# Optimization experiments

Measured on AMD Instinct MI355X. Metric: run time of the kernel, lower is better.

## Reference

```python
import jax, jax.numpy as jnp
import numpy as np

B, T, C, H = 2, 2048, 1024, 16
WINDOW = 512
SOFTCAP = 30.0


def setup_inputs() -> dict:
    key = jax.random.key(0)
    ks = jax.random.split(key, 4)
    s = 0.02
    return {
        "x": jax.random.normal(ks[0], (B, T, C), dtype=jnp.float32),
        "suffix_prefix_length": jax.random.randint(ks[1], (B,), 0, 256),
        "W_qkv": jax.random.normal(ks[2], (3 * C, C), dtype=jnp.float32) * s,
        "b_qkv": jnp.zeros((3 * C,), dtype=jnp.float32),
        "W_proj": jax.random.normal(ks[3], (C, C), dtype=jnp.float32) * s,
        "b_proj": jnp.zeros((C,), dtype=jnp.float32),
    }


def reference(x, suffix_prefix_length, W_qkv, b_qkv, W_proj, b_proj):
    Bb, Tt, Cc = x.shape
    d = Cc // H
    # fused qkv projection (torch Linear: x @ W.T + b)
    qkv = x @ W_qkv.T + b_qkv
    q, k, v = jnp.split(qkv, 3, axis=-1)
    q = q.reshape(Bb, Tt, H, d).transpose(0, 2, 1, 3)  # [B,H,T,d]
    k = k.reshape(Bb, Tt, H, d).transpose(0, 2, 1, 3)
    v = v.reshape(Bb, Tt, H, d).transpose(0, 2, 1, 3)

    scale = 1.0 / np.sqrt(d).astype(np.float32)
    scores = jnp.einsum("bhqd,bhkd->bhqk", q, k) * scale
    # tanh softcap applied to unmasked scores (flex_attention score_mod path)
    scores = jnp.tanh(scores / SOFTCAP) * SOFTCAP

    qi = jnp.arange(Tt)[:, None]
    kj = jnp.arange(Tt)[None, :]
    sliding_causal = (qi >= kj) & (qi - kj <= WINDOW)          # [T,T]
    prefix_global = kj[None, :, :] < suffix_prefix_length[:, None, None]  # [B,T,T]
    mask = sliding_causal[None, None, :, :] | prefix_global[:, None, :, :]

    scores = jnp.where(mask, scores, -jnp.inf)
    att = jax.nn.softmax(scores, axis=-1)
    y = jnp.einsum("bhqk,bhkd->bhqd", att, v)
    y = y.transpose(0, 2, 1, 3).reshape(Bb, Tt, Cc)
    return y @ W_proj.T + b_proj
```

## Files before the change

kernel.cpp:

```cpp
#include <hip/hip_runtime.h>
#include <hip/hip_bf16.h>

typedef __bf16 bf16x8 __attribute__((ext_vector_type(8)));
typedef float f32x4 __attribute__((ext_vector_type(4)));

#define DEVI __device__ __forceinline__

constexpr int B_ = 2, T_ = 2048, C_ = 1024, H_ = 16, D_ = 64;
constexpr int M_ = B_ * T_;
constexpr int K_ = C_;
constexpr int WINDOW_ = 512;

DEVI unsigned short f2bf(float f) {
  return __builtin_bit_cast(unsigned short, (__bf16)f);
}

DEVI void gl_lds16(const unsigned short* g, unsigned short* l) {
  __builtin_amdgcn_global_load_lds(
      (const __attribute__((address_space(1))) unsigned int*)g,
      (__attribute__((address_space(3))) unsigned int*)l, 16, 0, 0);
}

__global__ void cvt_all(const float* __restrict__ x, const float* __restrict__ wqkv,
                        const float* __restrict__ wproj,
                        unsigned short* __restrict__ xb,
                        unsigned short* __restrict__ wqkvb,
                        unsigned short* __restrict__ wprojb) {
  constexpr int N1 = M_ * K_ / 4, N2 = 3 * C_ * K_ / 4, N3 = C_ * K_ / 4;
  int i = blockIdx.x * blockDim.x + threadIdx.x;
  const float* in;
  unsigned short* out;
  int idx;
  if (i < N1) { in = x; out = xb; idx = i; }
  else if (i < N1 + N2) { in = wqkv; out = wqkvb; idx = i - N1; }
  else if (i < N1 + N2 + N3) { in = wproj; out = wprojb; idx = i - N1 - N2; }
  else return;
  float4 v = reinterpret_cast<const float4*>(in)[idx];
  ushort4 o;
  o.x = f2bf(v.x); o.y = f2bf(v.y); o.z = f2bf(v.z); o.w = f2bf(v.w);
  reinterpret_cast<ushort4*>(out)[idx] = o;
}

template <int WHICH>
__global__ __launch_bounds__(256) void gemm_bt(
    const unsigned short* __restrict__ A, const unsigned short* __restrict__ W,
    const float* __restrict__ bias,
    unsigned short* __restrict__ oq, unsigned short* __restrict__ ok,
    unsigned short* __restrict__ ov, float* __restrict__ of) {
  __shared__ alignas(16) unsigned short As[128 * 32];
  __shared__ alignas(16) unsigned short Bs[128 * 32];

  const int tid = threadIdx.x;
  const int n0 = blockIdx.x * 128, m0 = blockIdx.y * 128;
  const int lane = tid & 63, w = tid >> 6;
  const int wm = (w >> 1) * 64, wn = (w & 1) * 64;
  const int lr = lane & 15, lg = lane >> 4;
  const int srow = lane >> 2, scs = (lane & 3) << 3;

  f32x4 acc[4][4];
#pragma unroll
  for (int i = 0; i < 4; i++)
#pragma unroll
    for (int j = 0; j < 4; j++) acc[i][j] = f32x4{0.f, 0.f, 0.f, 0.f};

  for (int kt = 0; kt < K_; kt += 32) {
#pragma unroll
    for (int i = 0; i < 2; i++) {
      const int rb = i * 64 + w * 16;
      gl_lds16(&A[(size_t)(m0 + rb + srow) * K_ + kt + scs], &As[rb * 32]);
      gl_lds16(&W[(size_t)(n0 + rb + srow) * K_ + kt + scs], &Bs[rb * 32]);
    }
    __syncthreads();
    bf16x8 af[4], bfr[4];
#pragma unroll
    for (int m = 0; m < 4; m++)
      af[m] = *reinterpret_cast<const bf16x8*>(&As[(wm + m * 16 + lr) * 32 + lg * 8]);
#pragma unroll
    for (int n = 0; n < 4; n++)
      bfr[n] = *reinterpret_cast<const bf16x8*>(&Bs[(wn + n * 16 + lr) * 32 + lg * 8]);
#pragma unroll
    for (int m = 0; m < 4; m++)
#pragma unroll
      for (int n = 0; n < 4; n++)
        acc[m][n] = __builtin_amdgcn_mfma_f32_16x16x32_bf16(af[m], bfr[n], acc[m][n], 0, 0, 0);
    __syncthreads();
  }

#pragma unroll
  for (int ms = 0; ms < 4; ms++) {
#pragma unroll
    for (int ns = 0; ns < 4; ns++) {
#pragma unroll
      for (int r = 0; r < 4; r++) {
        int m = m0 + wm + ms * 16 + lg * 4 + r;
        int n = n0 + wn + ns * 16 + lr;
        if constexpr (WHICH == 0) {
          float v = acc[ms][ns][r] + bias[n];
          int part = n >> 10, nc = n & 1023;
          int hh = nc >> 6, dd = nc & 63;
          int bb = m >> 11, tt = m & 2047;
          unsigned short bv = f2bf(v);
          size_t addr = (((size_t)(bb * H_ + hh)) * T_ + tt) * D_ + dd;
          if (part == 0) oq[addr] = bv;
          else if (part == 1) ok[addr] = bv;
          else ov[addr] = bv;
        } else {
          of[(size_t)m * C_ + n] = acc[ms][ns][r] + bias[n];
        }
      }
    }
  }
}

__global__ __launch_bounds__(256) void attn_fwd(
    const unsigned short* __restrict__ qg, const unsigned short* __restrict__ kg,
    const unsigned short* __restrict__ vg, const int* __restrict__ spl_arr,
    unsigned short* __restrict__ out) {
  const int tid = threadIdx.x;
  const int l = tid & 63, w = tid >> 6;
  const int lr = l & 15, lg = l >> 4;

  constexpr float C1 = 0.012022458674074695f;
  constexpr float C3 = -86.56170245333781f;

  const int lin = blockIdx.x;
  const int xs = lin & 7, slot = lin >> 3;
  const int g = xs + 8 * (slot >> 5);
  const int iblk = slot & 31;
  const int b = g >> 4, h = g & 15;
  const int q_base = iblk * 64;
  const int i0 = q_base + w * 16;

  const int spl = spl_arr[b];
  const size_t bh = (size_t)(b * H_ + h);
  const unsigned short* qp = qg + bh * T_ * D_;
  const unsigned short* kp = kg + bh * T_ * D_;
  const unsigned short* vp = vg + bh * T_ * D_;

  __shared__ alignas(16) unsigned short Ks[64 * 64];
  __shared__ alignas(16) unsigned short Vs[64 * 64];
  __shared__ alignas(16) unsigned short Ps[4][16][80];

  bf16x8 aq0 = *reinterpret_cast<const bf16x8*>(qp + (size_t)(i0 + lr) * D_ + lg * 8);
  bf16x8 aq1 = *reinterpret_cast<const bf16x8*>(qp + (size_t)(i0 + lr) * D_ + 32 + lg * 8);

  const unsigned short one_bf = 0x3F80;
  bf16x8 ONES;
#pragma unroll
  for (int i = 0; i < 8; i++) ONES[i] = __builtin_bit_cast(__bf16, one_bf);

  f32x4 acc[4];
  f32x4 accl = f32x4{0.f, 0.f, 0.f, 0.f};
#pragma unroll
  for (int nb = 0; nb < 4; nb++) acc[nb] = f32x4{0.f, 0.f, 0.f, 0.f};

  const int pref_tiles = (spl + 63) >> 6;
  const int pref_end = pref_tiles << 6;
  int wl = q_base - WINDOW_; if (wl < 0) wl = 0; wl &= ~63;
  const int start2 = wl > pref_end ? wl : pref_end;
  const int hi = q_base + 63;
  const int n2 = (start2 <= hi) ? (((hi - start2) >> 6) + 1) : 0;
  const int ntot = pref_tiles + n2;

  const int strow = tid >> 2;
  const int c0 = (tid & 3) << 4;
  const int ssw = (strow & 7) << 3;

  for (int tb = 0; tb < ntot; tb++) {
    const int j0 = (tb < pref_tiles) ? (tb << 6) : (start2 + ((tb - pref_tiles) << 6));
    {
      const unsigned short* krow = kp + (size_t)(j0 + strow) * D_;
      int4 ka0 = *reinterpret_cast<const int4*>(krow + c0);
      int4 ka1 = *reinterpret_cast<const int4*>(krow + c0 + 8);
      *reinterpret_cast<int4*>(&Ks[strow * 64 + (c0 ^ ssw)]) = ka0;
      *reinterpret_cast<int4*>(&Ks[strow * 64 + ((c0 + 8) ^ ssw)]) = ka1;
      union { int4 v4[2]; unsigned short u[16]; } vv;
      const unsigned short* vrow = vp + (size_t)(j0 + l) * D_ + w * 16;
      vv.v4[0] = *reinterpret_cast<const int4*>(vrow);
      vv.v4[1] = *reinterpret_cast<const int4*>(vrow + 8);
#pragma unroll
      for (int e = 0; e < 16; e++) {
        const int d = w * 16 + e;
        Vs[d * 64 + (l ^ ((d & 7) << 3))] = vv.u[e];
      }
    }
    __syncthreads();

    const bool rel = (j0 < spl) || (j0 + 63 >= i0 - WINDOW_ && j0 <= i0 + 15);
    if (rel) {
      f32x4 s[4];
#pragma unroll
      for (int ks = 0; ks < 4; ks++) {
        const int krow = ks * 16 + lr;
        const int sw = (krow & 7) << 3;
        bf16x8 b0 = *reinterpret_cast<const bf16x8*>(&Ks[krow * 64 + ((lg * 8) ^ sw)]);
        bf16x8 b1 = *reinterpret_cast<const bf16x8*>(&Ks[krow * 64 + ((32 + lg * 8) ^ sw)]);
        f32x4 t = f32x4{0.f, 0.f, 0.f, 0.f};
        t = __builtin_amdgcn_mfma_f32_16x16x32_bf16(aq0, b0, t, 0, 0, 0);
        s[ks] = __builtin_amdgcn_mfma_f32_16x16x32_bf16(aq1, b1, t, 0, 0, 0);
      }

      const bool fullv = (j0 + 63 < spl) ||
                         ((j0 + 63 <= i0) && (i0 + 15 - j0 <= WINDOW_));
      if (fullv) {
#pragma unroll
        for (int r = 0; r < 4; r++) {
          const int prow = lg * 4 + r;
#pragma unroll
          for (int ks = 0; ks < 4; ks++) {
            float t = __builtin_amdgcn_exp2f(s[ks][r] * C1);
            float p = __builtin_amdgcn_exp2f(C3 * __builtin_amdgcn_rcpf(1.0f + t));
            Ps[w][prow][ks * 16 + lr] = f2bf(p);
          }
        }
      } else {
#pragma unroll
        for (int r = 0; r < 4; r++) {
          const int prow = lg * 4 + r;
          const int irow = i0 + prow;
#pragma unroll
          for (int ks = 0; ks < 4; ks++) {
            const int jc = j0 + ks * 16 + lr;
            float t = __builtin_amdgcn_exp2f(s[ks][r] * C1);
            float p = __builtin_amdgcn_exp2f(C3 * __builtin_amdgcn_rcpf(1.0f + t));
            bool valid = (jc <= irow && irow - jc <= WINDOW_) || (jc < spl);
            p = valid ? p : 0.0f;
            Ps[w][prow][ks * 16 + lr] = f2bf(p);
          }
        }
      }

      asm volatile("s_waitcnt lgkmcnt(0)" ::: "memory");

      bf16x8 pa0 = *reinterpret_cast<const bf16x8*>(&Ps[w][lr][lg * 8]);
      bf16x8 pa1 = *reinterpret_cast<const bf16x8*>(&Ps[w][lr][32 + lg * 8]);

      accl = __builtin_amdgcn_mfma_f32_16x16x32_bf16(pa0, ONES, accl, 0, 0, 0);
      accl = __builtin_amdgcn_mfma_f32_16x16x32_bf16(pa1, ONES, accl, 0, 0, 0);

#pragma unroll
      for (int nb = 0; nb < 4; nb++) {
        const int vrow = nb * 16 + lr;
        const int sw = (vrow & 7) << 3;
        bf16x8 bv0 = *reinterpret_cast<const bf16x8*>(&Vs[vrow * 64 + ((lg * 8) ^ sw)]);
        bf16x8 bv1 = *reinterpret_cast<const bf16x8*>(&Vs[vrow * 64 + ((32 + lg * 8) ^ sw)]);
        acc[nb] = __builtin_amdgcn_mfma_f32_16x16x32_bf16(pa0, bv0, acc[nb], 0, 0, 0);
        acc[nb] = __builtin_amdgcn_mfma_f32_16x16x32_bf16(pa1, bv1, acc[nb], 0, 0, 0);
      }
    }
    __syncthreads();
  }

  float rl[4];
#pragma unroll
  for (int r = 0; r < 4; r++) rl[r] = __builtin_amdgcn_rcpf(accl[r]);
#pragma unroll
  for (int nb = 0; nb < 4; nb++) {
#pragma unroll
    for (int r = 0; r < 4; r++) {
      float o = acc[nb][r] * rl[r];
      int t = i0 + lg * 4 + r;
      out[((size_t)(b * T_ + t)) * C_ + h * D_ + nb * 16 + lr] = f2bf(o);
    }
  }
}

extern "C" void kernel_launch(void* const* d_in, const int* in_sizes, int n_in,
                              void* d_out, int out_size, void* d_ws, size_t ws_size,
                              hipStream_t stream) {
  const float* x = (const float*)d_in[0];
  const int* spl = (const int*)d_in[1];
  const float* Wqkv = (const float*)d_in[2];
  const float* bqkv = (const float*)d_in[3];
  const float* Wproj = (const float*)d_in[4];
  const float* bproj = (const float*)d_in[5];
  float* out = (float*)d_out;

  char* ws = (char*)d_ws;
  unsigned short* xb = (unsigned short*)ws;       ws += (size_t)M_ * K_ * 2;
  unsigned short* wqkvb = (unsigned short*)ws;    ws += (size_t)3 * C_ * K_ * 2;
  unsigned short* wprojb = (unsigned short*)ws;   ws += (size_t)C_ * K_ * 2;
  unsigned short* qb = (unsigned short*)ws;       ws += (size_t)M_ * C_ * 2;
  unsigned short* kb = (unsigned short*)ws;       ws += (size_t)M_ * C_ * 2;
  unsigned short* vb = (unsigned short*)ws;       ws += (size_t)M_ * C_ * 2;
  unsigned short* ab = (unsigned short*)ws;       ws += (size_t)M_ * C_ * 2;

  {
    constexpr int NT = (M_ * K_ + 3 * C_ * K_ + C_ * K_) / 4;
    cvt_all<<<(NT + 255) / 256, 256, 0, stream>>>(x, Wqkv, Wproj, xb, wqkvb, wprojb);
  }

  gemm_bt<0><<<dim3(3072 / 128, M_ / 128), 256, 0, stream>>>(
      xb, wqkvb, bqkv, qb, kb, vb, nullptr);

  attn_fwd<<<dim3(1024), 256, 0, stream>>>(qb, kb, vb, spl, ab);

  gemm_bt<1><<<dim3(C_ / 128, M_ / 128), 256, 0, stream>>>(
      ab, wprojb, bproj, nullptr, nullptr, nullptr, out);
}
```

Before: 178.2 us.

## Replace GEMM with 256x256 double-buffered tile kernel using swizzled LDS

Replaces the 128x128, K=32 single-buffered GEMM with a 512-thread kernel. Each block computes a 256x256 tile with a K step of 64, and LDS is double-buffered so the next tile loads while the current one is multiplied, using explicit vmcnt waits. LDS columns are XOR-swizzled to avoid bank conflicts, and the block index is remapped to improve L2 locality. The larger tiles raise data reuse per block but shrink the grid to 192 and 64 blocks, which leaves many CUs idle, especially for the output projection. The 128KB of LDS also limits each CU to one block.

Measured after the change: 187.3 us. 1.05x slower.

```diff
diff --git a/kernel.cpp b/kernel.cpp
--- a/kernel.cpp
+++ b/kernel.cpp
@@ -42,60 +42,101 @@
 }
 
 template <int WHICH>
-__global__ __launch_bounds__(256) void gemm_bt(
+__global__ __launch_bounds__(512, 2) void gemm256(
     const unsigned short* __restrict__ A, const unsigned short* __restrict__ W,
     const float* __restrict__ bias,
     unsigned short* __restrict__ oq, unsigned short* __restrict__ ok,
     unsigned short* __restrict__ ov, float* __restrict__ of) {
-  __shared__ alignas(16) unsigned short As[128 * 32];
-  __shared__ alignas(16) unsigned short Bs[128 * 32];
+  constexpr int NK = K_ / 64;
+  __shared__ alignas(16) unsigned short Al[2][256 * 64];
+  __shared__ alignas(16) unsigned short Bl[2][256 * 64];
 
   const int tid = threadIdx.x;
-  const int n0 = blockIdx.x * 128, m0 = blockIdx.y * 128;
   const int lane = tid & 63, w = tid >> 6;
-  const int wm = (w >> 1) * 64, wn = (w & 1) * 64;
+
+  const int nbx = gridDim.x;
+  const int nwg = nbx * 16;
+  const int orig = blockIdx.y * nbx + blockIdx.x;
+  const int cpx = nwg >> 3;
+  const int swz = (orig & 7) * cpx + (orig >> 3);
+  const int m0 = (swz & 15) * 256;
+  const int n0 = (swz >> 4) * 256;
+
+  const int wm = (w >> 2) * 128;
+  const int wn = (w & 3) * 64;
   const int lr = lane & 15, lg = lane >> 4;
-  const int srow = lane >> 2, scs = (lane & 3) << 3;
-
-  f32x4 acc[4][4];
-#pragma unroll
-  for (int i = 0; i < 4; i++)
+
+  const int srow8 = lane >> 3;
+  const int scol = ((lane & 7) ^ srow8) << 3;
+
+  f32x4 acc[8][4];
+#pragma unroll
+  for (int i = 0; i < 8; i++)
 #pragma unroll
     for (int j = 0; j < 4; j++) acc[i][j] = f32x4{0.f, 0.f, 0.f, 0.f};
 
-  for (int kt = 0; kt < K_; kt += 32) {
-#pragma unroll
-    for (int i = 0; i < 2; i++) {
-      const int rb = i * 64 + w * 16;
-      gl_lds16(&A[(size_t)(m0 + rb + srow) * K_ + kt + scs], &As[rb * 32]);
-      gl_lds16(&W[(size_t)(n0 + rb + srow) * K_ + kt + scs], &Bs[rb * 32]);
-    }
-    __syncthreads();
-    bf16x8 af[4], bfr[4];
-#pragma unroll
-    for (int m = 0; m < 4; m++)
-      af[m] = *reinterpret_cast<const bf16x8*>(&As[(wm + m * 16 + lr) * 32 + lg * 8]);
-#pragma unroll
-    for (int n = 0; n < 4; n++)
-      bfr[n] = *reinterpret_cast<const bf16x8*>(&Bs[(wn + n * 16 + lr) * 32 + lg * 8]);
-#pragma unroll
-    for (int m = 0; m < 4; m++)
-#pragma unroll
-      for (int n = 0; n < 4; n++)
-        acc[m][n] = __builtin_amdgcn_mfma_f32_16x16x32_bf16(af[m], bfr[n], acc[m][n], 0, 0, 0);
-    __syncthreads();
-  }
-
-#pragma unroll
-  for (int ms = 0; ms < 4; ms++) {
-#pragma unroll
-    for (int ns = 0; ns < 4; ns++) {
+  auto ISSUE = [&](int kt, int b) {
+#pragma unroll
+    for (int i = 0; i < 4; i++) {
+      const int row = i * 64 + w * 8 + srow8;
+      gl_lds16(&A[(size_t)(m0 + row) * K_ + kt * 64 + scol],
+               &Al[b][(i * 64 + w * 8) * 64]);
+    }
+#pragma unroll
+    for (int i = 0; i < 4; i++) {
+      const int row = i * 64 + w * 8 + srow8;
+      gl_lds16(&W[(size_t)(n0 + row) * K_ + kt * 64 + scol],
+               &Bl[b][(i * 64 + w * 8) * 64]);
+    }
+  };
+
+  ISSUE(0, 0);
+  ISSUE(1, 1);
+
+  for (int kt = 0; kt < NK; kt++) {
+    const int b = kt & 1;
+    if (kt + 1 < NK) asm volatile("s_waitcnt vmcnt(8)" ::: "memory");
+    else             asm volatile("s_waitcnt vmcnt(0)" ::: "memory");
+    __builtin_amdgcn_s_barrier();
+
+    bf16x8 bfrag[4][2];
+#pragma unroll
+    for (int nf = 0; nf < 4; nf++)
+#pragma unroll
+      for (int ks = 0; ks < 2; ks++) {
+        const int row = wn + nf * 16 + lr;
+        const int c16 = (ks * 4 + lg) ^ (row & 7);
+        bfrag[nf][ks] = *reinterpret_cast<const bf16x8*>(&Bl[b][row * 64 + c16 * 8]);
+      }
+#pragma unroll
+    for (int mf = 0; mf < 8; mf++) {
+      const int row = wm + mf * 16 + lr;
+      const int c0 = (0 * 4 + lg) ^ (row & 7);
+      const int c1 = (1 * 4 + lg) ^ (row & 7);
+      bf16x8 af0 = *reinterpret_cast<const bf16x8*>(&Al[b][row * 64 + c0 * 8]);
+      bf16x8 af1 = *reinterpret_cast<const bf16x8*>(&Al[b][row * 64 + c1 * 8]);
+#pragma unroll
+      for (int nf = 0; nf < 4; nf++) {
+        acc[mf][nf] = __builtin_amdgcn_mfma_f32_16x16x32_bf16(af0, bfrag[nf][0], acc[mf][nf], 0, 0, 0);
+        acc[mf][nf] = __builtin_amdgcn_mfma_f32_16x16x32_bf16(af1, bfrag[nf][1], acc[mf][nf], 0, 0, 0);
+      }
+    }
+
+    asm volatile("s_waitcnt lgkmcnt(0)" ::: "memory");
+    __builtin_amdgcn_s_barrier();
+    if (kt + 2 < NK) ISSUE(kt + 2, b);
+  }
+
+#pragma unroll
+  for (int mf = 0; mf < 8; mf++) {
+#pragma unroll
+    for (int nf = 0; nf < 4; nf++) {
 #pragma unroll
       for (int r = 0; r < 4; r++) {
-        int m = m0 + wm + ms * 16 + lg * 4 + r;
-        int n = n0 + wn + ns * 16 + lr;
+        const int m = m0 + wm + mf * 16 + lg * 4 + r;
+        const int n = n0 + wn + nf * 16 + lr;
         if constexpr (WHICH == 0) {
-          float v = acc[ms][ns][r] + bias[n];
+          float v = acc[mf][nf][r] + bias[n];
           int part = n >> 10, nc = n & 1023;
           int hh = nc >> 6, dd = nc & 63;
           int bb = m >> 11, tt = m & 2047;
@@ -105,7 +146,7 @@
           else if (part == 1) ok[addr] = bv;
           else ov[addr] = bv;
         } else {
-          of[(size_t)m * C_ + n] = acc[ms][ns][r] + bias[n];
+          of[(size_t)m * C_ + n] = acc[mf][nf][r] + bias[n];
         }
       }
     }
@@ -290,11 +331,11 @@
     cvt_all<<<(NT + 255) / 256, 256, 0, stream>>>(x, Wqkv, Wproj, xb, wqkvb, wprojb);
   }
 
-  gemm_bt<0><<<dim3(3072 / 128, M_ / 128), 256, 0, stream>>>(
+  gemm256<0><<<dim3(3072 / 256, M_ / 256), 512, 0, stream>>>(
       xb, wqkvb, bqkv, qb, kb, vb, nullptr);
 
   attn_fwd<<<dim3(1024), 256, 0, stream>>>(qb, kb, vb, spl, ab);
 
-  gemm_bt<1><<<dim3(C_ / 128, M_ / 128), 256, 0, stream>>>(
+  gemm256<1><<<dim3(C_ / 256, M_ / 256), 512, 0, stream>>>(
       ab, wprojb, bproj, nullptr, nullptr, nullptr, out);
 }
```

## Double GEMM K-tile with XOR-swizzled LDS and pack V transpose stores

Applied to the files above, without the earlier changes.

The projection GEMM now stages 64-wide K tiles instead of 32, halving the number of barrier pairs per K loop, and XOR-swizzles the LDS layout so fragment reads avoid bank conflicts. In the attention kernel, each thread loads two adjacent V rows and writes packed 32-bit pairs into the transposed V tile, replacing the scalar 16-bit scattered stores. This doubles GEMM LDS usage, which may reduce occupancy.

New measurement: 187.5 us. 1.05x slower.

```diff
diff --git a/kernel.cpp b/kernel.cpp
--- a/kernel.cpp
+++ b/kernel.cpp
@@ -47,15 +47,17 @@
     const float* __restrict__ bias,
     unsigned short* __restrict__ oq, unsigned short* __restrict__ ok,
     unsigned short* __restrict__ ov, float* __restrict__ of) {
-  __shared__ alignas(16) unsigned short As[128 * 32];
-  __shared__ alignas(16) unsigned short Bs[128 * 32];
+  __shared__ alignas(16) unsigned short As[128 * 64];
+  __shared__ alignas(16) unsigned short Bs[128 * 64];
 
   const int tid = threadIdx.x;
   const int n0 = blockIdx.x * 128, m0 = blockIdx.y * 128;
   const int lane = tid & 63, w = tid >> 6;
   const int wm = (w >> 1) * 64, wn = (w & 1) * 64;
   const int lr = lane & 15, lg = lane >> 4;
-  const int srow = lane >> 2, scs = (lane & 3) << 3;
+
+  const int srow = lane >> 3;
+  const int scol = ((lane & 7) ^ srow) << 3;
 
   f32x4 acc[4][4];
 #pragma unroll
@@ -63,26 +65,41 @@
 #pragma unroll
     for (int j = 0; j < 4; j++) acc[i][j] = f32x4{0.f, 0.f, 0.f, 0.f};
 
-  for (int kt = 0; kt < K_; kt += 32) {
-#pragma unroll
-    for (int i = 0; i < 2; i++) {
-      const int rb = i * 64 + w * 16;
-      gl_lds16(&A[(size_t)(m0 + rb + srow) * K_ + kt + scs], &As[rb * 32]);
-      gl_lds16(&W[(size_t)(n0 + rb + srow) * K_ + kt + scs], &Bs[rb * 32]);
+  for (int kt = 0; kt < K_; kt += 64) {
+#pragma unroll
+    for (int i = 0; i < 4; i++) {
+      const int rb = i * 32 + w * 8;
+      gl_lds16(&A[(size_t)(m0 + rb + srow) * K_ + kt + scol], &As[rb * 64]);
+    }
+#pragma unroll
+    for (int i = 0; i < 4; i++) {
+      const int rb = i * 32 + w * 8;
+      gl_lds16(&W[(size_t)(n0 + rb + srow) * K_ + kt + scol], &Bs[rb * 64]);
     }
     __syncthreads();
-    bf16x8 af[4], bfr[4];
-#pragma unroll
-    for (int m = 0; m < 4; m++)
-      af[m] = *reinterpret_cast<const bf16x8*>(&As[(wm + m * 16 + lr) * 32 + lg * 8]);
-#pragma unroll
-    for (int n = 0; n < 4; n++)
-      bfr[n] = *reinterpret_cast<const bf16x8*>(&Bs[(wn + n * 16 + lr) * 32 + lg * 8]);
-#pragma unroll
-    for (int m = 0; m < 4; m++)
-#pragma unroll
-      for (int n = 0; n < 4; n++)
-        acc[m][n] = __builtin_amdgcn_mfma_f32_16x16x32_bf16(af[m], bfr[n], acc[m][n], 0, 0, 0);
+
+    bf16x8 af[4][2], bfr[4][2];
+#pragma unroll
+    for (int m = 0; m < 4; m++) {
+      const int row = wm + m * 16 + lr;
+      const int s = row & 7;
+      af[m][0] = *reinterpret_cast<const bf16x8*>(&As[row * 64 + ((lg ^ s) << 3)]);
+      af[m][1] = *reinterpret_cast<const bf16x8*>(&As[row * 64 + (((lg + 4) ^ s) << 3)]);
+    }
+#pragma unroll
+    for (int n = 0; n < 4; n++) {
+      const int row = wn + n * 16 + lr;
+      const int s = row & 7;
+      bfr[n][0] = *reinterpret_cast<const bf16x8*>(&Bs[row * 64 + ((lg ^ s) << 3)]);
+      bfr[n][1] = *reinterpret_cast<const bf16x8*>(&Bs[row * 64 + (((lg + 4) ^ s) << 3)]);
+    }
+#pragma unroll
+    for (int ks = 0; ks < 2; ks++)
+#pragma unroll
+      for (int m = 0; m < 4; m++)
+#pragma unroll
+        for (int n = 0; n < 4; n++)
+          acc[m][n] = __builtin_amdgcn_mfma_f32_16x16x32_bf16(af[m][ks], bfr[n][ks], acc[m][n], 0, 0, 0);
     __syncthreads();
   }
 
@@ -165,6 +182,7 @@
   const int strow = tid >> 2;
   const int c0 = (tid & 3) << 4;
   const int ssw = (strow & 7) << 3;
+  const int vpr = tid & 31, vc = tid >> 5;
 
   for (int tb = 0; tb < ntot; tb++) {
     const int j0 = (tb < pref_tiles) ? (tb << 6) : (start2 + ((tb - pref_tiles) << 6));
@@ -174,14 +192,14 @@
       int4 ka1 = *reinterpret_cast<const int4*>(krow + c0 + 8);
       *reinterpret_cast<int4*>(&Ks[strow * 64 + (c0 ^ ssw)]) = ka0;
       *reinterpret_cast<int4*>(&Ks[strow * 64 + ((c0 + 8) ^ ssw)]) = ka1;
-      union { int4 v4[2]; unsigned short u[16]; } vv;
-      const unsigned short* vrow = vp + (size_t)(j0 + l) * D_ + w * 16;
-      vv.v4[0] = *reinterpret_cast<const int4*>(vrow);
-      vv.v4[1] = *reinterpret_cast<const int4*>(vrow + 8);
-#pragma unroll
-      for (int e = 0; e < 16; e++) {
-        const int d = w * 16 + e;
-        Vs[d * 64 + (l ^ ((d & 7) << 3))] = vv.u[e];
+      union { int4 q4; unsigned short u[8]; } r0, r1;
+      r0.q4 = *reinterpret_cast<const int4*>(vp + (size_t)(j0 + 2 * vpr) * D_ + vc * 8);
+      r1.q4 = *reinterpret_cast<const int4*>(vp + (size_t)(j0 + 2 * vpr + 1) * D_ + vc * 8);
+#pragma unroll
+      for (int e = 0; e < 8; e++) {
+        const int d = vc * 8 + e;
+        unsigned pk = (unsigned)r0.u[e] | ((unsigned)r1.u[e] << 16);
+        *reinterpret_cast<unsigned*>(&Vs[d * 64 + ((2 * vpr) ^ ((d & 7) << 3))]) = pk;
       }
     }
     __syncthreads();
```
